# Kernel optimization log

Hardware: AMD Instinct MI355X
Metric: run time of the kernel (lower is better)

The kernel has to match this reference:

```python
import jax, jax.numpy as jnp
import numpy as np
import math

B, S, D, H = 2, 2048, 1024, 16
DK = D // H


def setup_inputs() -> dict:
    key = jax.random.key(0)
    ks = jax.random.split(key, 5)
    scale = 0.02
    x = jax.random.normal(ks[0], (B, S, D), dtype=jnp.float32)
    wq = jax.random.normal(ks[1], (D, D), dtype=jnp.float32) * scale
    wk = jax.random.normal(ks[2], (D, D), dtype=jnp.float32) * scale
    wv = jax.random.normal(ks[3], (D, D), dtype=jnp.float32) * scale
    wo = jax.random.normal(ks[4], (D, D), dtype=jnp.float32) * scale
    bq = jnp.zeros((D,), jnp.float32)
    bk = jnp.zeros((D,), jnp.float32)
    bv = jnp.zeros((D,), jnp.float32)
    bo = jnp.zeros((D,), jnp.float32)
    # causal mask: mask==0 positions are filled with -inf in the original
    mask = jnp.tril(jnp.ones((S, S), dtype=bool))[None, None]  # [1,1,S,S]
    return {"x": x, "mask": mask, "wq": wq, "bq": bq, "wk": wk, "bk": bk,
            "wv": wv, "bv": bv, "wo": wo, "bo": bo}


def reference(x, mask, wq, bq, wk, bk, wv, bv, wo, bo):
    b, sl, d = x.shape
    # torch Linear: y = x @ W^T + b
    def proj(w, bias):
        y = jnp.einsum('bsd,ed->bse', x, w) + bias
        return y.reshape(b, sl, H, DK).transpose(0, 2, 1, 3)  # [B,H,S,DK]
    q = proj(wq, bq)
    k = proj(wk, bk)
    v = proj(wv, bv)
    sc = jnp.einsum('bhqd,bhkd->bhqk', q, k) / math.sqrt(DK)  # [B,H,S,S]
    sc = jnp.where(mask, sc, -jnp.inf)
    aw = jax.nn.softmax(sc, axis=-1)
    # dropout is identity in eval mode (reference baseline)
    ao = jnp.einsum('bhqk,bhkd->bhqd', aw, v)
    ao = ao.transpose(0, 2, 1, 3).reshape(b, sl, d)
    out = jnp.einsum('bsd,ed->bse', ao, wo) + bo
    return out
```

## Files before the change

### kernel.cpp

```cpp
#include <hip/hip_runtime.h>
#include <cstdint>
#include <cstddef>

#define Bb 2
#define Ss 2048
#define Dd 1024
#define Hh 16
#define DKk 64

typedef unsigned short ushort_t;
typedef __bf16 bf16x8 __attribute__((ext_vector_type(8)));
typedef float f32x4 __attribute__((ext_vector_type(4)));
typedef unsigned short us8 __attribute__((ext_vector_type(8)));
typedef unsigned short us4 __attribute__((ext_vector_type(4)));

__device__ __forceinline__ ushort_t f2bf(float f) {
  __bf16 h = (__bf16)f;
  return __builtin_bit_cast(unsigned short, h);
}

__device__ __forceinline__ void gload_lds16(const void* g, void* l) {
  __builtin_amdgcn_global_load_lds(
      (__attribute__((address_space(1))) void*)(g),
      (__attribute__((address_space(3))) void*)(l),
      16, 0, 0);
}

__global__ __launch_bounds__(256) void cast_k(const float* __restrict__ s,
                                              ushort_t* __restrict__ d, int n8) {
  const int i = blockIdx.x * 256 + threadIdx.x;
  if (i >= n8) return;
  const float4* sp = (const float4*)s;
  float4 a = sp[2 * i], b = sp[2 * i + 1];
  us8 o;
  o[0] = f2bf(a.x); o[1] = f2bf(a.y); o[2] = f2bf(a.z); o[3] = f2bf(a.w);
  o[4] = f2bf(b.x); o[5] = f2bf(b.y); o[6] = f2bf(b.z); o[7] = f2bf(b.w);
  ((us8*)d)[i] = o;
}

template <int MODE>
__global__ __launch_bounds__(256) void gemm_k(
    const ushort_t* __restrict__ A, const ushort_t* __restrict__ W,
    const float* __restrict__ b0, const float* __restrict__ b1,
    const float* __restrict__ b2,
    ushort_t* __restrict__ oQ, ushort_t* __restrict__ oK,
    ushort_t* __restrict__ oVT, float* __restrict__ oF) {
  constexpr int Kd = 1024;
  __shared__ ushort_t As[128 * 32];
  __shared__ ushort_t Bs[128 * 32];
  const int tid = threadIdx.x;
  const int lane = tid & 63;
  const int wave = tid >> 6;
  const int m0 = blockIdx.y * 128;
  const int n0 = blockIdx.x * 128;
  const int lr = lane & 15;
  const int lg = lane >> 4;
  const int srow = lane >> 2;
  const int scol = (lane & 3) * 8;
  const int ar = (wave >> 1) * 64;
  const int bc = (wave & 1) * 64;

  f32x4 acc[4][4] = {};

  for (int kt = 0; kt < Kd / 32; ++kt) {
    const int k0 = kt * 32;
#pragma unroll
    for (int c = 0; c < 2; ++c) {
      const int seg = wave * 2 + c;
      const int row = seg * 16 + srow;
      gload_lds16(A + (size_t)(m0 + row) * Kd + k0 + scol, (char*)As + seg * 1024);
      gload_lds16(W + (size_t)(n0 + row) * Kd + k0 + scol, (char*)Bs + seg * 1024);
    }
    __syncthreads();
    bf16x8 af[4], bfr[4];
#pragma unroll
    for (int i = 0; i < 4; ++i)
      af[i] = *(const bf16x8*)&As[(ar + i * 16 + lr) * 32 + lg * 8];
#pragma unroll
    for (int j = 0; j < 4; ++j)
      bfr[j] = *(const bf16x8*)&Bs[(bc + j * 16 + lr) * 32 + lg * 8];
#pragma unroll
    for (int i = 0; i < 4; ++i)
#pragma unroll
      for (int j = 0; j < 4; ++j)
        acc[i][j] = __builtin_amdgcn_mfma_f32_16x16x32_bf16(af[i], bfr[j],
                                                            acc[i][j], 0, 0, 0);
    __syncthreads();
  }

#pragma unroll
  for (int i = 0; i < 4; ++i) {
    const int mrow = m0 + ar + i * 16 + lg * 4;
#pragma unroll
    for (int j = 0; j < 4; ++j) {
      const int n = n0 + bc + j * 16 + lr;
      if (MODE == 0) {
        const int sel = n >> 10;
        const int nn = n & 1023;
        const float bias = (sel == 0 ? b0 : sel == 1 ? b1 : b2)[nn];
        const int h = nn >> 6, dk = nn & 63;
        const int bidx = mrow >> 11;
        const int s = mrow & 2047;
        const int bh = bidx * Hh + h;
        if (sel == 2) {
          us4 pk;
#pragma unroll
          for (int r = 0; r < 4; ++r) pk[r] = f2bf(acc[i][j][r] + bias);
          *(us4*)&oVT[((size_t)bh * DKk + dk) * Ss + s] = pk;
        } else {
          ushort_t* dst = (sel == 0) ? oQ : oK;
          const float mul = (sel == 0) ? 0.125f : 1.0f;
#pragma unroll
          for (int r = 0; r < 4; ++r)
            dst[((size_t)bh * Ss + (s + r)) * DKk + dk] =
                f2bf((acc[i][j][r] + bias) * mul);
        }
      } else {
        const float bias = b0[n];
#pragma unroll
        for (int r = 0; r < 4; ++r)
          oF[(size_t)(mrow + r) * Dd + n] = acc[i][j][r] + bias;
      }
    }
  }
}

__global__ __launch_bounds__(256, 4) void attn_k(const ushort_t* __restrict__ Qg,
                                                 const ushort_t* __restrict__ Kg,
                                                 const ushort_t* __restrict__ Vt,
                                                 ushort_t* __restrict__ AO) {
  __shared__ ushort_t Ks[2][64 * 64];
  __shared__ ushort_t Pl[4][16 * 72];
  const int tid = threadIdx.x, lane = tid & 63, wave = tid >> 6;
  const int bx = blockIdx.x;
  const int r_ = bx >> 8;
  const int i_ = bx & 255;
  const int bh = i_ & 31;
  const int sub = i_ >> 5;
  const int g = 8 * r_ + ((r_ & 1) ? (7 - sub) : sub);
  const int lr = lane & 15, lg = lane >> 4;
  const ushort_t* Qp = Qg + (size_t)bh * Ss * DKk;
  const ushort_t* Kp = Kg + (size_t)bh * Ss * DKk;
  const ushort_t* Vp = Vt + (size_t)bh * DKk * Ss;
  ushort_t* P = Pl[wave];
  const int q0 = g * 64 + wave * 16;
  const int nt = g + 1;

  const int s_row = lane >> 3;
  const int s_slot = (lane & 7) ^ s_row;
  auto stageK = [&](int t, int buf) {
    const int j0t = t * 64;
    const int rb = wave * 16;
#pragma unroll
    for (int c = 0; c < 2; ++c) {
      gload_lds16(Kp + (size_t)(j0t + rb + c * 8 + s_row) * DKk + s_slot * 8,
                  &Ks[buf][(rb + c * 8) * 64]);
    }
  };

  stageK(0, 0);

  bf16x8 qf[2];
#pragma unroll
  for (int ks = 0; ks < 2; ++ks)
    qf[ks] = *(const bf16x8*)&Qp[(size_t)(q0 + lr) * DKk + ks * 32 + lg * 8];

  bf16x8 onesv;
#pragma unroll
  for (int e = 0; e < 8; ++e) onesv[e] = (__bf16)1.0f;

  f32x4 o[4] = {};
  f32x4 l4 = {};
  float m_[4];
#pragma unroll
  for (int r = 0; r < 4; ++r) m_[r] = -3e38f;

  __syncthreads();

  for (int t = 0; t < nt; ++t) {
    const int j0 = t * 64;
    const int cb = t & 1;
    if (t + 1 < nt) stageK(t + 1, cb ^ 1);
    bf16x8 vt[4][2];
#pragma unroll
    for (int dj = 0; dj < 4; ++dj)
#pragma unroll
      for (int ksp = 0; ksp < 2; ++ksp)
        vt[dj][ksp] = *(const bf16x8*)&Vp[(size_t)(dj * 16 + lr) * Ss + j0 +
                                          ksp * 32 + lg * 8];
    const bool diag = (t == nt - 1);
    const int ctmax = diag ? wave : 3;
    f32x4 sc[4];
    const int sw = lr & 7;
#pragma unroll
    for (int ct = 0; ct < 4; ++ct) {
      if (ct <= ctmax) {
        const int krow = ct * 16 + lr;
        const bf16x8 k0v = *(const bf16x8*)&Ks[cb][krow * 64 + ((lg ^ sw) * 8)];
        const bf16x8 k1v =
            *(const bf16x8*)&Ks[cb][krow * 64 + (((4 ^ lg) ^ sw) * 8)];
        f32x4 z = {};
        z = __builtin_amdgcn_mfma_f32_16x16x32_bf16(qf[0], k0v, z, 0, 0, 0);
        z = __builtin_amdgcn_mfma_f32_16x16x32_bf16(qf[1], k1v, z, 0, 0, 0);
        sc[ct] = z;
      } else {
        sc[ct] = (f32x4){-1e30f, -1e30f, -1e30f, -1e30f};
      }
    }
    if (diag) {
#pragma unroll
      for (int r = 0; r < 4; ++r)
        if (lr > lg * 4 + r) sc[wave][r] = -1e30f;
    }
    float fsc[4];
#pragma unroll
    for (int r = 0; r < 4; ++r) {
      float mx = fmaxf(fmaxf(sc[0][r], sc[1][r]), fmaxf(sc[2][r], sc[3][r]));
#pragma unroll
      for (int d = 1; d < 16; d <<= 1) mx = fmaxf(mx, __shfl_xor(mx, d, 64));
      const float mnew = fmaxf(m_[r], mx);
      fsc[r] = __expf(m_[r] - mnew);
      m_[r] = mnew;
#pragma unroll
      for (int ct = 0; ct < 4; ++ct)
        P[(lg * 4 + r) * 72 + ct * 16 + lr] = f2bf(__expf(sc[ct][r] - mnew));
    }
#pragma unroll
    for (int dj = 0; dj < 4; ++dj)
#pragma unroll
      for (int r = 0; r < 4; ++r) o[dj][r] *= fsc[r];
#pragma unroll
    for (int r = 0; r < 4; ++r) l4[r] *= fsc[r];
    asm volatile("s_waitcnt lgkmcnt(0)" ::: "memory");
    bf16x8 pa[2];
#pragma unroll
    for (int ksp = 0; ksp < 2; ++ksp)
      pa[ksp] = *(const bf16x8*)&P[lr * 72 + ksp * 32 + lg * 8];
    l4 = __builtin_amdgcn_mfma_f32_16x16x32_bf16(pa[0], onesv, l4, 0, 0, 0);
    l4 = __builtin_amdgcn_mfma_f32_16x16x32_bf16(pa[1], onesv, l4, 0, 0, 0);
#pragma unroll
    for (int dj = 0; dj < 4; ++dj)
#pragma unroll
      for (int ksp = 0; ksp < 2; ++ksp)
        o[dj] = __builtin_amdgcn_mfma_f32_16x16x32_bf16(pa[ksp], vt[dj][ksp],
                                                        o[dj], 0, 0, 0);
    __syncthreads();
  }
  const int bb = bh >> 4, hh = bh & 15;
#pragma unroll
  for (int r = 0; r < 4; ++r) {
    const float inv = 1.0f / l4[r];
    const size_t m = (size_t)bb * Ss + q0 + lg * 4 + r;
#pragma unroll
    for (int dj = 0; dj < 4; ++dj)
      AO[m * Dd + hh * 64 + dj * 16 + lr] = f2bf(o[dj][r] * inv);
  }
}

extern "C" void kernel_launch(void* const* d_in, const int* in_sizes, int n_in,
                              void* d_out, int out_size, void* d_ws, size_t ws_size,
                              hipStream_t stream) {
  const float* x  = (const float*)d_in[0];
  const float* wq = (const float*)d_in[2];
  const float* bq = (const float*)d_in[3];
  const float* wk = (const float*)d_in[4];
  const float* bk = (const float*)d_in[5];
  const float* wv = (const float*)d_in[6];
  const float* bv = (const float*)d_in[7];
  const float* wo = (const float*)d_in[8];
  const float* bo = (const float*)d_in[9];

  ushort_t* ws   = (ushort_t*)d_ws;
  ushort_t* xb   = ws;
  ushort_t* wqkv = xb + 4096 * 1024;
  ushort_t* wob  = wqkv + 3072 * 1024;
  ushort_t* Qb   = wob + 1024 * 1024;
  ushort_t* Kb   = Qb + 4194304;
  ushort_t* VTb  = Kb + 4194304;
  ushort_t* AOb  = xb;

  cast_k<<<2048, 256, 0, stream>>>(x, xb, 524288);
  cast_k<<<512, 256, 0, stream>>>(wq, wqkv, 131072);
  cast_k<<<512, 256, 0, stream>>>(wk, wqkv + 1048576, 131072);
  cast_k<<<512, 256, 0, stream>>>(wv, wqkv + 2097152, 131072);
  cast_k<<<512, 256, 0, stream>>>(wo, wob, 131072);

  gemm_k<0><<<dim3(24, 32), 256, 0, stream>>>(xb, wqkv, bq, bk, bv, Qb, Kb, VTb,
                                              nullptr);
  attn_k<<<1024, 256, 0, stream>>>(Qb, Kb, VTb, AOb);
  gemm_k<1><<<dim3(8, 32), 256, 0, stream>>>(AOb, wob, bo, nullptr, nullptr,
                                             nullptr, nullptr, nullptr,
                                             (float*)d_out);
}
```

Baseline: 152.8 us.

## Restructure attention: transposed S, register-resident P, exp2 softmax, paired causal tiles

Rewrites the attention kernel to compute S transposed (K as the A operand), so the probabilities stay in registers as the B operand of 16x16x16 MFMAs. This removes the per-wave LDS round trip for P and the ones-vector MFMA used for row sums. Q is pre-scaled by log2(e)/sqrt(dk) so softmax can use exp2. Blocks now have 2 waves over 32-query tiles and each block processes a short and a long causal tile, balancing work across blocks. In exchange, the V loads become narrower 8-byte reads and each block gets fewer waves.

```diff
diff --git a/kernel.cpp b/kernel.cpp
--- a/kernel.cpp
+++ b/kernel.cpp
@@ -10,6 +10,8 @@
 
 typedef unsigned short ushort_t;
 typedef __bf16 bf16x8 __attribute__((ext_vector_type(8)));
+typedef __bf16 bf16x4 __attribute__((ext_vector_type(4)));
+typedef short s16x4 __attribute__((ext_vector_type(4)));
 typedef float f32x4 __attribute__((ext_vector_type(4)));
 typedef unsigned short us8 __attribute__((ext_vector_type(8)));
 typedef unsigned short us4 __attribute__((ext_vector_type(4)));
@@ -18,6 +20,25 @@
   __bf16 h = (__bf16)f;
   return __builtin_bit_cast(unsigned short, h);
 }
+
+#if __has_builtin(__builtin_amdgcn_mfma_f32_16x16x16bf16_1k)
+__device__ __forceinline__ void mfma16(f32x4& c, bf16x4 a, bf16x4 b) {
+  c = __builtin_amdgcn_mfma_f32_16x16x16bf16_1k(
+      __builtin_bit_cast(s16x4, a), __builtin_bit_cast(s16x4, b), c, 0, 0, 0);
+}
+#elif __has_builtin(__builtin_amdgcn_mfma_f32_16x16x16_bf16)
+__device__ __forceinline__ void mfma16(f32x4& c, bf16x4 a, bf16x4 b) {
+  c = __builtin_amdgcn_mfma_f32_16x16x16_bf16(a, b, c, 0, 0, 0);
+}
+#else
+__device__ __forceinline__ void mfma16(f32x4& c, bf16x4 a, bf16x4 b) {
+  __builtin_amdgcn_sched_barrier(0);
+  asm volatile("s_nop 4\n\tv_mfma_f32_16x16x16_bf16 %0, %1, %2, %0\n\ts_nop 4"
+               : "+v"(c)
+               : "v"(a), "v"(b));
+  __builtin_amdgcn_sched_barrier(0);
+}
+#endif
 
 __device__ __forceinline__ void gload_lds16(const void* g, void* l) {
   __builtin_amdgcn_global_load_lds(
@@ -109,7 +130,7 @@
           *(us4*)&oVT[((size_t)bh * DKk + dk) * Ss + s] = pk;
         } else {
           ushort_t* dst = (sel == 0) ? oQ : oK;
-          const float mul = (sel == 0) ? 0.125f : 1.0f;
+          const float mul = (sel == 0) ? 0.1803368842f : 1.0f;
 #pragma unroll
           for (int r = 0; r < 4; ++r)
             dst[((size_t)bh * Ss + (s + r)) * DKk + dk] =
@@ -125,135 +146,151 @@
   }
 }
 
-__global__ __launch_bounds__(256, 4) void attn_k(const ushort_t* __restrict__ Qg,
+__global__ __launch_bounds__(128, 2) void attn_k(const ushort_t* __restrict__ Qg,
                                                  const ushort_t* __restrict__ Kg,
                                                  const ushort_t* __restrict__ Vt,
                                                  ushort_t* __restrict__ AO) {
   __shared__ ushort_t Ks[2][64 * 64];
-  __shared__ ushort_t Pl[4][16 * 72];
   const int tid = threadIdx.x, lane = tid & 63, wave = tid >> 6;
   const int bx = blockIdx.x;
-  const int r_ = bx >> 8;
-  const int i_ = bx & 255;
-  const int bh = i_ & 31;
-  const int sub = i_ >> 5;
-  const int g = 8 * r_ + ((r_ & 1) ? (7 - sub) : sub);
+  const int bh = bx & 31;
+  const int p_ = bx >> 5;
   const int lr = lane & 15, lg = lane >> 4;
   const ushort_t* Qp = Qg + (size_t)bh * Ss * DKk;
   const ushort_t* Kp = Kg + (size_t)bh * Ss * DKk;
   const ushort_t* Vp = Vt + (size_t)bh * DKk * Ss;
-  ushort_t* P = Pl[wave];
-  const int q0 = g * 64 + wave * 16;
-  const int nt = g + 1;
-
   const int s_row = lane >> 3;
   const int s_slot = (lane & 7) ^ s_row;
-  auto stageK = [&](int t, int buf) {
-    const int j0t = t * 64;
-    const int rb = wave * 16;
-#pragma unroll
-    for (int c = 0; c < 2; ++c) {
-      gload_lds16(Kp + (size_t)(j0t + rb + c * 8 + s_row) * DKk + s_slot * 8,
-                  &Ks[buf][(rb + c * 8) * 64]);
-    }
-  };
-
-  stageK(0, 0);
-
-  bf16x8 qf[2];
-#pragma unroll
-  for (int ks = 0; ks < 2; ++ks)
-    qf[ks] = *(const bf16x8*)&Qp[(size_t)(q0 + lr) * DKk + ks * 32 + lg * 8];
-
-  bf16x8 onesv;
-#pragma unroll
-  for (int e = 0; e < 8; ++e) onesv[e] = (__bf16)1.0f;
-
-  f32x4 o[4] = {};
-  f32x4 l4 = {};
-  float m_[4];
-#pragma unroll
-  for (int r = 0; r < 4; ++r) m_[r] = -3e38f;
-
-  __syncthreads();
-
-  for (int t = 0; t < nt; ++t) {
-    const int j0 = t * 64;
-    const int cb = t & 1;
-    if (t + 1 < nt) stageK(t + 1, cb ^ 1);
-    bf16x8 vt[4][2];
-#pragma unroll
-    for (int dj = 0; dj < 4; ++dj)
-#pragma unroll
-      for (int ksp = 0; ksp < 2; ++ksp)
-        vt[dj][ksp] = *(const bf16x8*)&Vp[(size_t)(dj * 16 + lr) * Ss + j0 +
-                                          ksp * 32 + lg * 8];
-    const bool diag = (t == nt - 1);
-    const int ctmax = diag ? wave : 3;
-    f32x4 sc[4];
-    const int sw = lr & 7;
-#pragma unroll
-    for (int ct = 0; ct < 4; ++ct) {
-      if (ct <= ctmax) {
-        const int krow = ct * 16 + lr;
-        const bf16x8 k0v = *(const bf16x8*)&Ks[cb][krow * 64 + ((lg ^ sw) * 8)];
-        const bf16x8 k1v =
-            *(const bf16x8*)&Ks[cb][krow * 64 + (((4 ^ lg) ^ sw) * 8)];
-        f32x4 z = {};
-        z = __builtin_amdgcn_mfma_f32_16x16x32_bf16(qf[0], k0v, z, 0, 0, 0);
-        z = __builtin_amdgcn_mfma_f32_16x16x32_bf16(qf[1], k1v, z, 0, 0, 0);
-        sc[ct] = z;
-      } else {
-        sc[ct] = (f32x4){-1e30f, -1e30f, -1e30f, -1e30f};
-      }
-    }
-    if (diag) {
-#pragma unroll
-      for (int r = 0; r < 4; ++r)
-        if (lr > lg * 4 + r) sc[wave][r] = -1e30f;
-    }
-    float fsc[4];
-#pragma unroll
-    for (int r = 0; r < 4; ++r) {
-      float mx = fmaxf(fmaxf(sc[0][r], sc[1][r]), fmaxf(sc[2][r], sc[3][r]));
-#pragma unroll
-      for (int d = 1; d < 16; d <<= 1) mx = fmaxf(mx, __shfl_xor(mx, d, 64));
-      const float mnew = fmaxf(m_[r], mx);
-      fsc[r] = __expf(m_[r] - mnew);
-      m_[r] = mnew;
+  const int bb = bh >> 4, hh = bh & 15;
+  const int sw = lr & 7;
+
+  for (int half = 0; half < 2; ++half) {
+    const int t32 = half ? (63 - p_) : p_;
+    const int nt = (t32 >> 1) + 1;
+    const int q0 = t32 * 32 + wave * 16;
+    const int ctmax = wave + ((t32 & 1) << 1);
+
+    {
+      const int rb = wave * 32;
+#pragma unroll
+      for (int c = 0; c < 4; ++c)
+        gload_lds16(Kp + (size_t)(c * 8 + rb + s_row) * DKk + s_slot * 8,
+                    &Ks[0][(rb + c * 8) * 64]);
+    }
+
+    bf16x8 qf[2];
+#pragma unroll
+    for (int ks = 0; ks < 2; ++ks)
+      qf[ks] = *(const bf16x8*)&Qp[(size_t)(q0 + lr) * DKk + ks * 32 + lg * 8];
+
+    f32x4 o[4] = {};
+    float m_ = -3e38f, l_ = 0.f;
+
+    __syncthreads();
+
+    for (int t = 0; t < nt; ++t) {
+      const int j0 = t * 64;
+      const int cb = t & 1;
+      if (t + 1 < nt) {
+        const int rb = wave * 32;
+#pragma unroll
+        for (int c = 0; c < 4; ++c)
+          gload_lds16(Kp + (size_t)((t + 1) * 64 + c * 8 + rb + s_row) * DKk +
+                          s_slot * 8,
+                      &Ks[cb ^ 1][(rb + c * 8) * 64]);
+      }
+      const bool diag = (t == nt - 1);
+      const int nct = diag ? ctmax + 1 : 4;
+
+      bf16x4 vt4[4][4];
 #pragma unroll
       for (int ct = 0; ct < 4; ++ct)
-        P[(lg * 4 + r) * 72 + ct * 16 + lr] = f2bf(__expf(sc[ct][r] - mnew));
-    }
-#pragma unroll
-    for (int dj = 0; dj < 4; ++dj)
-#pragma unroll
-      for (int r = 0; r < 4; ++r) o[dj][r] *= fsc[r];
-#pragma unroll
-    for (int r = 0; r < 4; ++r) l4[r] *= fsc[r];
-    asm volatile("s_waitcnt lgkmcnt(0)" ::: "memory");
-    bf16x8 pa[2];
-#pragma unroll
-    for (int ksp = 0; ksp < 2; ++ksp)
-      pa[ksp] = *(const bf16x8*)&P[lr * 72 + ksp * 32 + lg * 8];
-    l4 = __builtin_amdgcn_mfma_f32_16x16x32_bf16(pa[0], onesv, l4, 0, 0, 0);
-    l4 = __builtin_amdgcn_mfma_f32_16x16x32_bf16(pa[1], onesv, l4, 0, 0, 0);
-#pragma unroll
-    for (int dj = 0; dj < 4; ++dj)
-#pragma unroll
-      for (int ksp = 0; ksp < 2; ++ksp)
-        o[dj] = __builtin_amdgcn_mfma_f32_16x16x32_bf16(pa[ksp], vt[dj][ksp],
-                                                        o[dj], 0, 0, 0);
-    __syncthreads();
-  }
-  const int bb = bh >> 4, hh = bh & 15;
-#pragma unroll
-  for (int r = 0; r < 4; ++r) {
-    const float inv = 1.0f / l4[r];
-    const size_t m = (size_t)bb * Ss + q0 + lg * 4 + r;
-#pragma unroll
-    for (int dj = 0; dj < 4; ++dj)
-      AO[m * Dd + hh * 64 + dj * 16 + lr] = f2bf(o[dj][r] * inv);
+        if (ct < nct)
+#pragma unroll
+          for (int dj = 0; dj < 4; ++dj)
+            vt4[dj][ct] = *(const bf16x4*)&Vp[(size_t)(dj * 16 + lr) * Ss + j0 +
+                                              ct * 16 + lg * 4];
+
+      f32x4 sc[4];
+#pragma unroll
+      for (int ct = 0; ct < 4; ++ct) {
+        if (ct < nct) {
+          const int krow = ct * 16 + lr;
+          const bf16x8 k0v = *(const bf16x8*)&Ks[cb][krow * 64 + ((lg ^ sw) * 8)];
+          const bf16x8 k1v =
+              *(const bf16x8*)&Ks[cb][krow * 64 + (((4 | lg) ^ sw) * 8)];
+          f32x4 z = {};
+          z = __builtin_amdgcn_mfma_f32_16x16x32_bf16(k0v, qf[0], z, 0, 0, 0);
+          z = __builtin_amdgcn_mfma_f32_16x16x32_bf16(k1v, qf[1], z, 0, 0, 0);
+          sc[ct] = z;
+        }
+      }
+      if (diag) {
+#pragma unroll
+        for (int ct = 0; ct < 4; ++ct)
+          if (ct == nct - 1)
+#pragma unroll
+            for (int r = 0; r < 4; ++r)
+              if (lg * 4 + r > lr) sc[ct][r] = -1e30f;
+      }
+
+      float mx = -3e38f;
+#pragma unroll
+      for (int ct = 0; ct < 4; ++ct)
+        if (ct < nct)
+#pragma unroll
+          for (int r = 0; r < 4; ++r) mx = fmaxf(mx, sc[ct][r]);
+      mx = fmaxf(mx, __shfl_xor(mx, 16, 64));
+      mx = fmaxf(mx, __shfl_xor(mx, 32, 64));
+      const float mnew = fmaxf(m_, mx);
+      const float fs = __builtin_exp2f(m_ - mnew);
+      m_ = mnew;
+      float ls = 0.f;
+      bf16x4 pb[4];
+#pragma unroll
+      for (int ct = 0; ct < 4; ++ct) {
+        if (ct < nct) {
+          float p0 = __builtin_exp2f(sc[ct][0] - mnew);
+          float p1 = __builtin_exp2f(sc[ct][1] - mnew);
+          float p2 = __builtin_exp2f(sc[ct][2] - mnew);
+          float p3 = __builtin_exp2f(sc[ct][3] - mnew);
+          ls += (p0 + p1) + (p2 + p3);
+          bf16x4 pbv;
+          pbv[0] = (__bf16)p0;
+          pbv[1] = (__bf16)p1;
+          pbv[2] = (__bf16)p2;
+          pbv[3] = (__bf16)p3;
+          pb[ct] = pbv;
+        }
+      }
+      ls += __shfl_xor(ls, 16, 64);
+      ls += __shfl_xor(ls, 32, 64);
+      l_ = l_ * fs + ls;
+#pragma unroll
+      for (int dj = 0; dj < 4; ++dj)
+#pragma unroll
+        for (int r = 0; r < 4; ++r) o[dj][r] *= fs;
+
+      __builtin_amdgcn_s_setprio(1);
+#pragma unroll
+      for (int dj = 0; dj < 4; ++dj)
+#pragma unroll
+        for (int ct = 0; ct < 4; ++ct)
+          if (ct < nct) mfma16(o[dj], vt4[dj][ct], pb[ct]);
+      __builtin_amdgcn_s_setprio(0);
+
+      __syncthreads();
+    }
+
+    const float inv = 1.0f / l_;
+#pragma unroll
+    for (int dj = 0; dj < 4; ++dj) {
+      us4 pk;
+#pragma unroll
+      for (int r = 0; r < 4; ++r) pk[r] = f2bf(o[dj][r] * inv);
+      *(us4*)&AO[((size_t)bb * Ss + q0 + lr) * Dd + hh * 64 + dj * 16 + lg * 4] =
+          pk;
+    }
   }
 }
 
@@ -287,7 +324,7 @@
 
   gemm_k<0><<<dim3(24, 32), 256, 0, stream>>>(xb, wqkv, bq, bk, bv, Qb, Kb, VTb,
                                               nullptr);
-  attn_k<<<1024, 256, 0, stream>>>(Qb, Kb, VTb, AOb);
+  attn_k<<<1024, 128, 0, stream>>>(Qb, Kb, VTb, AOb);
   gemm_k<1><<<dim3(8, 32), 256, 0, stream>>>(AOb, wob, bo, nullptr, nullptr,
                                              nullptr, nullptr, nullptr,
                                              (float*)d_out);
```

Result: slower. 202.8 us (+32.7%).
